# Kernel optimization log

Measured on AMD Instinct MI355X. Metric: run time of the kernel, lower is better.

## Reference

```python
import jax, jax.numpy as jnp
import numpy as np

BS, C, H, W = 8, 128, 64, 64
CH = C // 2  # proj output channels


def setup_inputs() -> dict:
    key = jax.random.key(0)
    ks = jax.random.split(key, 8)
    s = 1.0 / np.sqrt(C)
    return {
        "tgt": jax.random.normal(ks[0], (BS, C, H, W), dtype=jnp.float32),
        "ref": jax.random.normal(ks[1], (BS, C, H, W), dtype=jnp.float32),
        "W_tgt": jax.random.normal(ks[2], (CH, C), dtype=jnp.float32) * s,
        "b_tgt": jax.random.normal(ks[3], (CH,), dtype=jnp.float32) * s,
        "W_ref": jax.random.normal(ks[4], (CH, C), dtype=jnp.float32) * s,
        "b_ref": jax.random.normal(ks[5], (CH,), dtype=jnp.float32) * s,
        "W_out": jax.random.normal(ks[6], (C, C), dtype=jnp.float32) * s,
        "b_out": jax.random.normal(ks[7], (C,), dtype=jnp.float32) * s,
    }


def reference(tgt, ref, W_tgt, b_tgt, W_ref, b_ref, W_out, b_out):
    bs, c, h, w = tgt.shape
    n = h * w
    # 1x1 conv == per-pixel matmul over channels; flatten spatial to tokens
    tgt_f = tgt.reshape(bs, c, n)              # [bs, c, n]
    ref_f = ref.reshape(bs, c, n)              # [bs, c, n]
    # att_tgt: [bs, n, c/2] ; att_ref: [bs, c/2, n] (ReLU after proj)
    att_tgt = jax.nn.relu(jnp.einsum('bcn,oc->bno', tgt_f, W_tgt) + b_tgt)
    att_ref = jax.nn.relu(jnp.einsum('bcn,oc->bon', ref_f, W_ref) + b_ref[None, :, None])
    pre_att = jnp.einsum('bnd,bdm->bnm', att_tgt, att_ref)   # [bs, n, n]
    att = jax.nn.softmax(pre_att, axis=-1)
    # fused tokens: [bs, n, c] = att @ ref_tokens
    fused = jnp.einsum('bnm,bcm->bnc', att, ref_f)
    fused = fused.transpose(0, 2, 1).reshape(bs, c, h, w)
    # output gate: 1x1 conv on tgt (no activation), elementwise mul
    att_out = jnp.einsum('bcn,oc->bon', tgt_f, W_out) + b_out[None, :, None]
    fused = fused * att_out.reshape(bs, c, h, w)
    return fused
```

## Files before the change

### kernel.cpp

```cpp
#include <hip/hip_runtime.h>

typedef __attribute__((ext_vector_type(8))) _Float16 f16x8;
typedef __attribute__((ext_vector_type(4))) float f32x4;

constexpr int kC  = 128;
constexpr int kCH = 64;
constexpr int kN  = 4096;
constexpr float kLog2e = 1.4426950408889634f;

__device__ __forceinline__ unsigned pkrtz(float a, float b) {
    union { __fp16 __attribute__((ext_vector_type(2))) v; unsigned u; } cv;
    cv.v = __builtin_amdgcn_cvt_pkrtz(a, b);
    return cv.u;
}

__device__ __forceinline__ float x2(float x) {
    return __builtin_amdgcn_exp2f(x);
}

__device__ __forceinline__ void g2l16(const unsigned short* g, unsigned short* l) {
    __builtin_amdgcn_global_load_lds(
        (const __attribute__((address_space(1))) unsigned int*)(g),
        (__attribute__((address_space(3))) unsigned int*)(l),
        16, 0, 0);
}

__global__ __launch_bounds__(256, 4) void proj_mfma(
    const float* __restrict__ tgt, const float* __restrict__ ref,
    const float* __restrict__ Wt, const float* __restrict__ Wr,
    const float* __restrict__ Wo, const float* __restrict__ bt,
    const float* __restrict__ br, const float* __restrict__ bo,
    unsigned short* __restrict__ Qw, unsigned short* __restrict__ Kw,
    unsigned short* __restrict__ Vw, float* __restrict__ Gw)
{
    __shared__ __align__(16) unsigned short Xs[64 * 128];
    const int t = threadIdx.x;
    const int slice = blockIdx.y >> 3;
    const int b = blockIdx.y & 7;
    const int tokb = blockIdx.x << 6;

    const int w = t >> 6, lane = t & 63;
    const int lg = (lane >> 4) & 3, lm = lane & 15;

    const float* X = (slice == 1) ? ref : tgt;
    const float* Xb = X + ((size_t)b * kC) * kN + tokb;
    unsigned short* Vout = Vw + ((size_t)b * kC) * kN + tokb;

    const int tk4 = (t & 15) * 4;
    const int c8  = (t >> 4) * 8;
    f32x4 xv[8];
    #pragma unroll
    for (int j = 0; j < 8; ++j)
        xv[j] = *(const f32x4*)(Xb + (size_t)(c8 + j) * kN + tk4);

    f16x8 wf[2][4];
    float bvv[2][4];
    if (slice == 2) {
        const int ocb = w * 32;
        #pragma unroll
        for (int ot = 0; ot < 2; ++ot) {
            const int oc = ocb + ot * 16 + lm;
            #pragma unroll
            for (int ks = 0; ks < 4; ++ks) {
                const float* wp = Wo + (size_t)oc * kC + ks * 32 + lg * 8;
                f32x4 f0 = *(const f32x4*)wp;
                f32x4 f1 = *(const f32x4*)(wp + 4);
                union { f16x8 h; uint4 u; } cv;
                cv.u = make_uint4(pkrtz(f0[0], f0[1]), pkrtz(f0[2], f0[3]),
                                  pkrtz(f1[0], f1[1]), pkrtz(f1[2], f1[3]));
                wf[ot][ks] = cv.h;
            }
            #pragma unroll
            for (int r = 0; r < 4; ++r) bvv[ot][r] = bo[ocb + ot * 16 + lg * 4 + r];
        }
    } else {
        const float* W    = slice ? Wr : Wt;
        const float* bias = slice ? br : bt;
        const float scale = slice ? 1.0f : kLog2e;
        const int ocb = w * 16;
        #pragma unroll
        for (int ks = 0; ks < 4; ++ks) {
            const float* wp = W + (size_t)(ocb + lm) * kC + ks * 32 + lg * 8;
            f32x4 f0 = *(const f32x4*)wp;
            f32x4 f1 = *(const f32x4*)(wp + 4);
            union { f16x8 h; uint4 u; } cv;
            cv.u = make_uint4(pkrtz(f0[0] * scale, f0[1] * scale),
                              pkrtz(f0[2] * scale, f0[3] * scale),
                              pkrtz(f1[0] * scale, f1[1] * scale),
                              pkrtz(f1[2] * scale, f1[3] * scale));
            wf[0][ks] = cv.h;
        }
        #pragma unroll
        for (int r = 0; r < 4; ++r) bvv[0][r] = bias[ocb + lg * 4 + r] * scale;
    }

    if (slice == 1) {
        #pragma unroll
        for (int j = 0; j < 8; ++j)
            *(uint2*)(Vout + (size_t)(c8 + j) * kN + tk4) =
                make_uint2(pkrtz(xv[j][0], xv[j][1]), pkrtz(xv[j][2], xv[j][3]));
    }
    #pragma unroll
    for (int s = 0; s < 4; ++s) {
        const int tok = tk4 + s;
        const int cc = (c8 >> 3) ^ (tok & 7);
        uint4 pk;
        pk.x = pkrtz(xv[0][s], xv[1][s]);
        pk.y = pkrtz(xv[2][s], xv[3][s]);
        pk.z = pkrtz(xv[4][s], xv[5][s]);
        pk.w = pkrtz(xv[6][s], xv[7][s]);
        *(uint4*)(Xs + tok * 128 + cc * 8) = pk;
    }
    __syncthreads();

    if (slice == 2) {
        const int ocb = w * 32;
        float* Gb = Gw + ((size_t)b * kC) * kN + tokb;
        #pragma unroll
        for (int ns = 0; ns < 4; ++ns) {
            const int tok = ns * 16 + lm;
            f16x8 xf[4];
            #pragma unroll
            for (int ks = 0; ks < 4; ++ks)
                xf[ks] = *(const f16x8*)(Xs + tok * 128 +
                                         (((ks * 4 + lg) ^ (tok & 7)) << 3));
            #pragma unroll
            for (int ot = 0; ot < 2; ++ot) {
                f32x4 acc = {bvv[ot][0], bvv[ot][1], bvv[ot][2], bvv[ot][3]};
                #pragma unroll
                for (int ks = 0; ks < 4; ++ks)
                    acc = __builtin_amdgcn_mfma_f32_16x16x32_f16(wf[ot][ks], xf[ks], acc, 0, 0, 0);
                #pragma unroll
                for (int r = 0; r < 4; ++r)
                    Gb[(size_t)(ocb + ot * 16 + lg * 4 + r) * kN + tok] = acc[r];
            }
        }
    } else {
        const int ocb = w * 16;
        unsigned short* outp = (slice ? Kw : Qw) + ((size_t)b * kN + tokb) * kCH;
        #pragma unroll
        for (int ns = 0; ns < 4; ++ns) {
            const int tok = ns * 16 + lm;
            f16x8 xf[4];
            #pragma unroll
            for (int ks = 0; ks < 4; ++ks)
                xf[ks] = *(const f16x8*)(Xs + tok * 128 +
                                         (((ks * 4 + lg) ^ (tok & 7)) << 3));
            f32x4 acc = {bvv[0][0], bvv[0][1], bvv[0][2], bvv[0][3]};
            #pragma unroll
            for (int ks = 0; ks < 4; ++ks)
                acc = __builtin_amdgcn_mfma_f32_16x16x32_f16(wf[0][ks], xf[ks], acc, 0, 0, 0);
            uint2 pk;
            pk.x = pkrtz(fmaxf(acc[0], 0.f), fmaxf(acc[1], 0.f));
            pk.y = pkrtz(fmaxf(acc[2], 0.f), fmaxf(acc[3], 0.f));
            *(uint2*)(outp + (size_t)tok * kCH + ocb + lg * 4) = pk;
        }
    }
}

__global__ __launch_bounds__(256, 2) void flash7_kernel(
    const unsigned short* __restrict__ Qw,
    const unsigned short* __restrict__ Kw,
    const unsigned short* __restrict__ Vw,
    const float* __restrict__ Gw,
    float* __restrict__ out)
{
    __shared__ __align__(16) unsigned short Ks[2][64 * 64];
    __shared__ __align__(16) unsigned short Vs[2][128 * 64];
    __shared__ __align__(16) unsigned short Ps[64 * 64];

    const int t = threadIdx.x;
    const int b = blockIdx.x & 7;
    const int n0 = (blockIdx.x >> 3) << 6;
    const int w = t >> 6, lane = t & 63;
    const int lg = (lane >> 4) & 3, lm = lane & 15;
    const int row_q = w * 16 + lm;
    const int swz = lm & 7;

    const unsigned short* Qb = Qw + ((size_t)b * kN) * kCH;
    const unsigned short* Kb = Kw + ((size_t)b * kN) * kCH;
    const unsigned short* Vb = Vw + ((size_t)b * kC) * kN;

    f16x8 qf0 = *(const f16x8*)(Qb + (size_t)(n0 + row_q) * kCH + (lg << 3));
    f16x8 qf1 = *(const f16x8*)(Qb + (size_t)(n0 + row_q) * kCH + 32 + (lg << 3));

    const int srow = t >> 3, scol = t & 7;
    const int sco  = (scol ^ (srow & 7)) << 3;
    const int wv   = t >> 6;

    const int fswz0 = (lg ^ swz) << 3;
    const int fswz1 = ((4 | lg) ^ swz) << 3;
    int psw[4];
    #pragma unroll
    for (int mb = 0; mb < 4; ++mb)
        psw[mb] = row_q * 64 + (((2 * mb + (lg >> 1)) ^ swz) << 3) + ((lg & 1) << 2);

    union { f16x8 h; uint4 u; } onec;
    onec.u = make_uint4(0x3c003c00u, 0x3c003c00u, 0x3c003c00u, 0x3c003c00u);
    const f16x8 onev = onec.h;

    f32x4 O[8];
    #pragma unroll
    for (int cb = 0; cb < 8; ++cb) O[cb] = (f32x4){0.f, 0.f, 0.f, 0.f};
    f32x4 L = (f32x4){0.f, 0.f, 0.f, 0.f};
    float m_run = 0.0f;

    unsigned short* Ks0 = Ks[0]; unsigned short* Ks1 = Ks[1];
    unsigned short* Vs0 = Vs[0]; unsigned short* Vs1 = Vs[1];

    auto stage = [&](unsigned short* Kd, unsigned short* Vd, int m0) {
        g2l16(Kb + (size_t)(m0 + srow) * kCH + sco,      Kd + wv * 512);
        g2l16(Kb + (size_t)(m0 + 32 + srow) * kCH + sco, Kd + 2048 + wv * 512);
        #pragma unroll
        for (int j = 0; j < 4; ++j)
            g2l16(Vb + (size_t)(32 * j + srow) * kN + m0 + sco,
                  Vd + j * 2048 + wv * 512);
    };
    stage(Ks0, Vs0, 0);

    auto tile = [&](const unsigned short* Kc, const unsigned short* Vc,
                    unsigned short* Kn, unsigned short* Vn, int kt) {
        __syncthreads();
        if (kt + 1 < kN / 64) stage(Kn, Vn, (kt + 1) << 6);

        f32x4 s[4];
        __builtin_amdgcn_s_setprio(1);
        #pragma unroll
        for (int mb = 0; mb < 4; ++mb) {
            const unsigned short* kr = Kc + ((mb * 16 + lm) << 6);
            f16x8 kf0 = *(const f16x8*)(kr + fswz0);
            f16x8 kf1 = *(const f16x8*)(kr + fswz1);
            f32x4 acc = (f32x4){0.f, 0.f, 0.f, 0.f};
            acc = __builtin_amdgcn_mfma_f32_16x16x32_f16(kf0, qf0, acc, 0, 0, 0);
            acc = __builtin_amdgcn_mfma_f32_16x16x32_f16(kf1, qf1, acc, 0, 0, 0);
            s[mb] = acc;
        }
        __builtin_amdgcn_s_setprio(0);

        float mloc = 0.0f;
        #pragma unroll
        for (int mb = 0; mb < 4; ++mb)
            #pragma unroll
            for (int r = 0; r < 4; ++r) mloc = fmaxf(mloc, s[mb][r]);
        mloc = fmaxf(mloc, __shfl_xor(mloc, 16, 64));
        mloc = fmaxf(mloc, __shfl_xor(mloc, 32, 64));
        const bool upd = __any(mloc > m_run);
        const float mnew = upd ? fmaxf(m_run, mloc) : m_run;

        #pragma unroll
        for (int mb = 0; mb < 4; ++mb) {
            unsigned plo = pkrtz(x2(s[mb][0] - mnew), x2(s[mb][1] - mnew));
            unsigned phi = pkrtz(x2(s[mb][2] - mnew), x2(s[mb][3] - mnew));
            *(uint2*)(Ps + psw[mb]) = make_uint2(plo, phi);
        }

        if (upd) {
            float alpha = x2(m_run - mnew);
            float a0 = __shfl(alpha, (lg << 2) + 0, 64);
            float a1 = __shfl(alpha, (lg << 2) + 1, 64);
            float a2 = __shfl(alpha, (lg << 2) + 2, 64);
            float a3 = __shfl(alpha, (lg << 2) + 3, 64);
            #pragma unroll
            for (int cb = 0; cb < 8; ++cb) {
                O[cb][0] *= a0; O[cb][1] *= a1; O[cb][2] *= a2; O[cb][3] *= a3;
            }
            L[0] *= a0; L[1] *= a1; L[2] *= a2; L[3] *= a3;
            m_run = mnew;
        }

        f16x8 pf0 = *(const f16x8*)(Ps + row_q * 64 + fswz0);
        f16x8 pf1 = *(const f16x8*)(Ps + row_q * 64 + fswz1);
        __builtin_amdgcn_s_setprio(1);
        L = __builtin_amdgcn_mfma_f32_16x16x32_f16(pf0, onev, L, 0, 0, 0);
        L = __builtin_amdgcn_mfma_f32_16x16x32_f16(pf1, onev, L, 0, 0, 0);
        #pragma unroll
        for (int cb = 0; cb < 8; ++cb) {
            const unsigned short* vr = Vc + ((cb * 16 + lm) << 6);
            f16x8 vf0 = *(const f16x8*)(vr + fswz0);
            f16x8 vf1 = *(const f16x8*)(vr + fswz1);
            O[cb] = __builtin_amdgcn_mfma_f32_16x16x32_f16(pf0, vf0, O[cb], 0, 0, 0);
            O[cb] = __builtin_amdgcn_mfma_f32_16x16x32_f16(pf1, vf1, O[cb], 0, 0, 0);
        }
        __builtin_amdgcn_s_setprio(0);
    };

    for (int kt = 0; kt < kN / 64; kt += 2) {
        tile(Ks0, Vs0, Ks1, Vs1, kt);
        tile(Ks1, Vs1, Ks0, Vs0, kt + 1);
    }

    const float i0 = 1.0f / L[0], i1 = 1.0f / L[1];
    const float i2 = 1.0f / L[2], i3 = 1.0f / L[3];
    const float* Gb = Gw + ((size_t)b * kC) * kN;
    float* Ob = out + ((size_t)b * kC) * kN;
    #pragma unroll
    for (int cb = 0; cb < 8; ++cb) {
        int c = cb * 16 + lm;
        size_t base = (size_t)c * kN + n0 + w * 16 + (lg << 2);
        float4 g = *(const float4*)(Gb + base);
        float4 res;
        res.x = O[cb][0] * i0 * g.x;
        res.y = O[cb][1] * i1 * g.y;
        res.z = O[cb][2] * i2 * g.z;
        res.w = O[cb][3] * i3 * g.w;
        *(float4*)(Ob + base) = res;
    }
}

extern "C" void kernel_launch(void* const* d_in, const int* in_sizes, int n_in,
                              void* d_out, int out_size, void* d_ws, size_t ws_size,
                              hipStream_t stream) {
    const float* tgt   = (const float*)d_in[0];
    const float* ref   = (const float*)d_in[1];
    const float* W_tgt = (const float*)d_in[2];
    const float* b_tgt = (const float*)d_in[3];
    const float* W_ref = (const float*)d_in[4];
    const float* b_ref = (const float*)d_in[5];
    const float* W_out = (const float*)d_in[6];
    const float* b_out = (const float*)d_in[7];
    float* out = (float*)d_out;

    const size_t QK = (size_t)8 * kN * kCH;
    const size_t CV = (size_t)8 * kC * kN;
    unsigned short* Qw = (unsigned short*)d_ws;
    unsigned short* Kw = Qw + QK;
    unsigned short* Vw = Kw + QK;
    float*          Gw = (float*)(Vw + CV);

    proj_mfma<<<dim3(64, 24), 256, 0, stream>>>(tgt, ref, W_tgt, W_ref, W_out,
                                                b_tgt, b_ref, b_out, Qw, Kw, Vw, Gw);
    flash7_kernel<<<dim3(512), 256, 0, stream>>>(Qw, Kw, Vw, Gw, out);
}
```

Measured before the change: 186.8 us.

## Fuse Q and gate projections over shared tgt tile and double-buffer token tiles

```diff
diff --git a/kernel.cpp b/kernel.cpp
--- a/kernel.cpp
+++ b/kernel.cpp
@@ -25,7 +25,7 @@
         16, 0, 0);
 }
 
-__global__ __launch_bounds__(256, 4) void proj_mfma(
+__global__ __launch_bounds__(256, 2) void proj_fused(
     const float* __restrict__ tgt, const float* __restrict__ ref,
     const float* __restrict__ Wt, const float* __restrict__ Wr,
     const float* __restrict__ Wo, const float* __restrict__ bt,
@@ -33,29 +33,46 @@
     unsigned short* __restrict__ Qw, unsigned short* __restrict__ Kw,
     unsigned short* __restrict__ Vw, float* __restrict__ Gw)
 {
-    __shared__ __align__(16) unsigned short Xs[64 * 128];
+    __shared__ __align__(16) unsigned short Xs[2][64 * 128];
     const int t = threadIdx.x;
-    const int slice = blockIdx.y >> 3;
+    const int sl2 = blockIdx.y >> 3;
     const int b = blockIdx.y & 7;
-    const int tokb = blockIdx.x << 6;
+    const int tok0 = blockIdx.x << 7;
 
     const int w = t >> 6, lane = t & 63;
     const int lg = (lane >> 4) & 3, lm = lane & 15;
 
-    const float* X = (slice == 1) ? ref : tgt;
-    const float* Xb = X + ((size_t)b * kC) * kN + tokb;
-    unsigned short* Vout = Vw + ((size_t)b * kC) * kN + tokb;
-
-    const int tk4 = (t & 15) * 4;
-    const int c8  = (t >> 4) * 8;
-    f32x4 xv[8];
-    #pragma unroll
-    for (int j = 0; j < 8; ++j)
-        xv[j] = *(const f32x4*)(Xb + (size_t)(c8 + j) * kN + tk4);
-
-    f16x8 wf[2][4];
-    float bvv[2][4];
-    if (slice == 2) {
+    const float* X = sl2 ? ref : tgt;
+    const float* Xb0 = X + ((size_t)b * kC) * kN + tok0;
+    unsigned short* Vout = Vw + ((size_t)b * kC) * kN + tok0;
+
+    const float* Wqk  = sl2 ? Wr : Wt;
+    const float* bqk  = sl2 ? br : bt;
+    const float scale = sl2 ? 1.0f : kLog2e;
+
+    f16x8 wfq[4];
+    float bq[4];
+    {
+        const int ocb = w * 16;
+        #pragma unroll
+        for (int ks = 0; ks < 4; ++ks) {
+            const float* wp = Wqk + (size_t)(ocb + lm) * kC + ks * 32 + lg * 8;
+            f32x4 f0 = *(const f32x4*)wp;
+            f32x4 f1 = *(const f32x4*)(wp + 4);
+            union { f16x8 h; uint4 u; } cv;
+            cv.u = make_uint4(pkrtz(f0[0] * scale, f0[1] * scale),
+                              pkrtz(f0[2] * scale, f0[3] * scale),
+                              pkrtz(f1[0] * scale, f1[1] * scale),
+                              pkrtz(f1[2] * scale, f1[3] * scale));
+            wfq[ks] = cv.h;
+        }
+        #pragma unroll
+        for (int r = 0; r < 4; ++r) bq[r] = bqk[ocb + lg * 4 + r] * scale;
+    }
+
+    f16x8 wfg[2][4];
+    float bg[2][4];
+    if (sl2 == 0) {
         const int ocb = w * 32;
         #pragma unroll
         for (int ot = 0; ot < 2; ++ot) {
@@ -68,94 +85,87 @@
                 union { f16x8 h; uint4 u; } cv;
                 cv.u = make_uint4(pkrtz(f0[0], f0[1]), pkrtz(f0[2], f0[3]),
                                   pkrtz(f1[0], f1[1]), pkrtz(f1[2], f1[3]));
-                wf[ot][ks] = cv.h;
+                wfg[ot][ks] = cv.h;
             }
             #pragma unroll
-            for (int r = 0; r < 4; ++r) bvv[ot][r] = bo[ocb + ot * 16 + lg * 4 + r];
-        }
-    } else {
-        const float* W    = slice ? Wr : Wt;
-        const float* bias = slice ? br : bt;
-        const float scale = slice ? 1.0f : kLog2e;
-        const int ocb = w * 16;
-        #pragma unroll
-        for (int ks = 0; ks < 4; ++ks) {
-            const float* wp = W + (size_t)(ocb + lm) * kC + ks * 32 + lg * 8;
-            f32x4 f0 = *(const f32x4*)wp;
-            f32x4 f1 = *(const f32x4*)(wp + 4);
-            union { f16x8 h; uint4 u; } cv;
-            cv.u = make_uint4(pkrtz(f0[0] * scale, f0[1] * scale),
-                              pkrtz(f0[2] * scale, f0[3] * scale),
-                              pkrtz(f1[0] * scale, f1[1] * scale),
-                              pkrtz(f1[2] * scale, f1[3] * scale));
-            wf[0][ks] = cv.h;
-        }
-        #pragma unroll
-        for (int r = 0; r < 4; ++r) bvv[0][r] = bias[ocb + lg * 4 + r] * scale;
+            for (int r = 0; r < 4; ++r) bg[ot][r] = bo[ocb + ot * 16 + lg * 4 + r];
+        }
     }
 
-    if (slice == 1) {
+    const int tk4 = (t & 15) * 4;
+    const int c8  = (t >> 4) * 8;
+
+    auto loadX = [&](int toff, f32x4* xv) {
         #pragma unroll
         for (int j = 0; j < 8; ++j)
-            *(uint2*)(Vout + (size_t)(c8 + j) * kN + tk4) =
-                make_uint2(pkrtz(xv[j][0], xv[j][1]), pkrtz(xv[j][2], xv[j][3]));
-    }
-    #pragma unroll
-    for (int s = 0; s < 4; ++s) {
-        const int tok = tk4 + s;
-        const int cc = (c8 >> 3) ^ (tok & 7);
-        uint4 pk;
-        pk.x = pkrtz(xv[0][s], xv[1][s]);
-        pk.y = pkrtz(xv[2][s], xv[3][s]);
-        pk.z = pkrtz(xv[4][s], xv[5][s]);
-        pk.w = pkrtz(xv[6][s], xv[7][s]);
-        *(uint4*)(Xs + tok * 128 + cc * 8) = pk;
-    }
-    __syncthreads();
-
-    if (slice == 2) {
-        const int ocb = w * 32;
+            xv[j] = *(const f32x4*)(Xb0 + (size_t)(c8 + j) * kN + toff + tk4);
+    };
+    auto stageX = [&](const f32x4* xv, unsigned short* Xsb, int toff) {
+        if (sl2 == 1) {
+            #pragma unroll
+            for (int j = 0; j < 8; ++j)
+                *(uint2*)(Vout + (size_t)(c8 + j) * kN + toff + tk4) =
+                    make_uint2(pkrtz(xv[j][0], xv[j][1]), pkrtz(xv[j][2], xv[j][3]));
+        }
+        #pragma unroll
+        for (int s = 0; s < 4; ++s) {
+            const int tok = tk4 + s;
+            const int cc = (c8 >> 3) ^ (tok & 7);
+            uint4 pk;
+            pk.x = pkrtz(xv[0][s], xv[1][s]);
+            pk.y = pkrtz(xv[2][s], xv[3][s]);
+            pk.z = pkrtz(xv[4][s], xv[5][s]);
+            pk.w = pkrtz(xv[6][s], xv[7][s]);
+            *(uint4*)(Xsb + tok * 128 + cc * 8) = pk;
+        }
+    };
+    auto compute = [&](const unsigned short* Xsb, int tokb) {
+        unsigned short* outp = (sl2 ? Kw : Qw) + ((size_t)b * kN + tokb) * kCH;
         float* Gb = Gw + ((size_t)b * kC) * kN + tokb;
+        const int ocq = w * 16;
+        const int ocg = w * 32;
         #pragma unroll
         for (int ns = 0; ns < 4; ++ns) {
             const int tok = ns * 16 + lm;
             f16x8 xf[4];
             #pragma unroll
             for (int ks = 0; ks < 4; ++ks)
-                xf[ks] = *(const f16x8*)(Xs + tok * 128 +
+                xf[ks] = *(const f16x8*)(Xsb + tok * 128 +
                                          (((ks * 4 + lg) ^ (tok & 7)) << 3));
-            #pragma unroll
-            for (int ot = 0; ot < 2; ++ot) {
-                f32x4 acc = {bvv[ot][0], bvv[ot][1], bvv[ot][2], bvv[ot][3]};
+            {
+                f32x4 acc = {bq[0], bq[1], bq[2], bq[3]};
                 #pragma unroll
                 for (int ks = 0; ks < 4; ++ks)
-                    acc = __builtin_amdgcn_mfma_f32_16x16x32_f16(wf[ot][ks], xf[ks], acc, 0, 0, 0);
+                    acc = __builtin_amdgcn_mfma_f32_16x16x32_f16(wfq[ks], xf[ks], acc, 0, 0, 0);
+                uint2 pk;
+                pk.x = pkrtz(fmaxf(acc[0], 0.f), fmaxf(acc[1], 0.f));
+                pk.y = pkrtz(fmaxf(acc[2], 0.f), fmaxf(acc[3], 0.f));
+                *(uint2*)(outp + (size_t)tok * kCH + ocq + lg * 4) = pk;
+            }
+            if (sl2 == 0) {
                 #pragma unroll
-                for (int r = 0; r < 4; ++r)
-                    Gb[(size_t)(ocb + ot * 16 + lg * 4 + r) * kN + tok] = acc[r];
+                for (int ot = 0; ot < 2; ++ot) {
+                    f32x4 acc = {bg[ot][0], bg[ot][1], bg[ot][2], bg[ot][3]};
+                    #pragma unroll
+                    for (int ks = 0; ks < 4; ++ks)
+                        acc = __builtin_amdgcn_mfma_f32_16x16x32_f16(wfg[ot][ks], xf[ks], acc, 0, 0, 0);
+                    #pragma unroll
+                    for (int r = 0; r < 4; ++r)
+                        Gb[(size_t)(ocg + ot * 16 + lg * 4 + r) * kN + tok] = acc[r];
+                }
             }
         }
-    } else {
-        const int ocb = w * 16;
-        unsigned short* outp = (slice ? Kw : Qw) + ((size_t)b * kN + tokb) * kCH;
-        #pragma unroll
-        for (int ns = 0; ns < 4; ++ns) {
-            const int tok = ns * 16 + lm;
-            f16x8 xf[4];
-            #pragma unroll
-            for (int ks = 0; ks < 4; ++ks)
-                xf[ks] = *(const f16x8*)(Xs + tok * 128 +
-                                         (((ks * 4 + lg) ^ (tok & 7)) << 3));
-            f32x4 acc = {bvv[0][0], bvv[0][1], bvv[0][2], bvv[0][3]};
-            #pragma unroll
-            for (int ks = 0; ks < 4; ++ks)
-                acc = __builtin_amdgcn_mfma_f32_16x16x32_f16(wf[0][ks], xf[ks], acc, 0, 0, 0);
-            uint2 pk;
-            pk.x = pkrtz(fmaxf(acc[0], 0.f), fmaxf(acc[1], 0.f));
-            pk.y = pkrtz(fmaxf(acc[2], 0.f), fmaxf(acc[3], 0.f));
-            *(uint2*)(outp + (size_t)tok * kCH + ocb + lg * 4) = pk;
-        }
-    }
+    };
+
+    f32x4 xv[8], xw[8];
+    loadX(0, xv);
+    stageX(xv, Xs[0], 0);
+    __syncthreads();
+    loadX(64, xw);
+    compute(Xs[0], tok0);
+    stageX(xw, Xs[1], 64);
+    __syncthreads();
+    compute(Xs[1], tok0 + 64);
 }
 
 __global__ __launch_bounds__(256, 2) void flash7_kernel(
@@ -327,7 +337,7 @@
     unsigned short* Vw = Kw + QK;
     float*          Gw = (float*)(Vw + CV);
 
-    proj_mfma<<<dim3(64, 24), 256, 0, stream>>>(tgt, ref, W_tgt, W_ref, W_out,
-                                                b_tgt, b_ref, b_out, Qw, Kw, Vw, Gw);
+    proj_fused<<<dim3(32, 16), 256, 0, stream>>>(tgt, ref, W_tgt, W_ref, W_out,
+                                                 b_tgt, b_ref, b_out, Qw, Kw, Vw, Gw);
     flash7_kernel<<<dim3(512), 256, 0, stream>>>(Qw, Kw, Vw, Gw, out);
 }
```

Result: no change. 183.4 us (-1.8%).

## Fuse query projection and output gate into flash attention kernel

Applied to the files above, without the earlier changes.

```diff
diff --git a/kernel.cpp b/kernel.cpp
--- a/kernel.cpp
+++ b/kernel.cpp
@@ -25,25 +25,26 @@
         16, 0, 0);
 }
 
-__global__ __launch_bounds__(256, 4) void proj_mfma(
-    const float* __restrict__ tgt, const float* __restrict__ ref,
-    const float* __restrict__ Wt, const float* __restrict__ Wr,
-    const float* __restrict__ Wo, const float* __restrict__ bt,
-    const float* __restrict__ br, const float* __restrict__ bo,
-    unsigned short* __restrict__ Qw, unsigned short* __restrict__ Kw,
-    unsigned short* __restrict__ Vw, float* __restrict__ Gw)
+__device__ __forceinline__ void lds_barrier() {
+    asm volatile("s_waitcnt lgkmcnt(0)" ::: "memory");
+    __builtin_amdgcn_sched_barrier(0);
+    __builtin_amdgcn_s_barrier();
+}
+
+__global__ __launch_bounds__(256, 2) void proj_kv(
+    const float* __restrict__ ref, const float* __restrict__ Wr,
+    const float* __restrict__ br, unsigned short* __restrict__ Kw,
+    unsigned short* __restrict__ Vw)
 {
     __shared__ __align__(16) unsigned short Xs[64 * 128];
     const int t = threadIdx.x;
-    const int slice = blockIdx.y >> 3;
-    const int b = blockIdx.y & 7;
+    const int b = blockIdx.y;
     const int tokb = blockIdx.x << 6;
 
     const int w = t >> 6, lane = t & 63;
     const int lg = (lane >> 4) & 3, lm = lane & 15;
 
-    const float* X = (slice == 1) ? ref : tgt;
-    const float* Xb = X + ((size_t)b * kC) * kN + tokb;
+    const float* Xb = ref + ((size_t)b * kC) * kN + tokb;
     unsigned short* Vout = Vw + ((size_t)b * kC) * kN + tokb;
 
     const int tk4 = (t & 15) * 4;
@@ -53,53 +54,26 @@
     for (int j = 0; j < 8; ++j)
         xv[j] = *(const f32x4*)(Xb + (size_t)(c8 + j) * kN + tk4);
 
-    f16x8 wf[2][4];
-    float bvv[2][4];
-    if (slice == 2) {
-        const int ocb = w * 32;
-        #pragma unroll
-        for (int ot = 0; ot < 2; ++ot) {
-            const int oc = ocb + ot * 16 + lm;
-            #pragma unroll
-            for (int ks = 0; ks < 4; ++ks) {
-                const float* wp = Wo + (size_t)oc * kC + ks * 32 + lg * 8;
-                f32x4 f0 = *(const f32x4*)wp;
-                f32x4 f1 = *(const f32x4*)(wp + 4);
-                union { f16x8 h; uint4 u; } cv;
-                cv.u = make_uint4(pkrtz(f0[0], f0[1]), pkrtz(f0[2], f0[3]),
-                                  pkrtz(f1[0], f1[1]), pkrtz(f1[2], f1[3]));
-                wf[ot][ks] = cv.h;
-            }
-            #pragma unroll
-            for (int r = 0; r < 4; ++r) bvv[ot][r] = bo[ocb + ot * 16 + lg * 4 + r];
-        }
-    } else {
-        const float* W    = slice ? Wr : Wt;
-        const float* bias = slice ? br : bt;
-        const float scale = slice ? 1.0f : kLog2e;
-        const int ocb = w * 16;
-        #pragma unroll
-        for (int ks = 0; ks < 4; ++ks) {
-            const float* wp = W + (size_t)(ocb + lm) * kC + ks * 32 + lg * 8;
-            f32x4 f0 = *(const f32x4*)wp;
-            f32x4 f1 = *(const f32x4*)(wp + 4);
-            union { f16x8 h; uint4 u; } cv;
-            cv.u = make_uint4(pkrtz(f0[0] * scale, f0[1] * scale),
-                              pkrtz(f0[2] * scale, f0[3] * scale),
-                              pkrtz(f1[0] * scale, f1[1] * scale),
-                              pkrtz(f1[2] * scale, f1[3] * scale));
-            wf[0][ks] = cv.h;
-        }
-        #pragma unroll
-        for (int r = 0; r < 4; ++r) bvv[0][r] = bias[ocb + lg * 4 + r] * scale;
-    }
-
-    if (slice == 1) {
-        #pragma unroll
-        for (int j = 0; j < 8; ++j)
-            *(uint2*)(Vout + (size_t)(c8 + j) * kN + tk4) =
-                make_uint2(pkrtz(xv[j][0], xv[j][1]), pkrtz(xv[j][2], xv[j][3]));
-    }
+    f16x8 wf[4];
+    float bq[4];
+    const int ocb = w * 16;
+    #pragma unroll
+    for (int ks = 0; ks < 4; ++ks) {
+        const float* wp = Wr + (size_t)(ocb + lm) * kC + ks * 32 + lg * 8;
+        f32x4 f0 = *(const f32x4*)wp;
+        f32x4 f1 = *(const f32x4*)(wp + 4);
+        union { f16x8 h; uint4 u; } cv;
+        cv.u = make_uint4(pkrtz(f0[0], f0[1]), pkrtz(f0[2], f0[3]),
+                          pkrtz(f1[0], f1[1]), pkrtz(f1[2], f1[3]));
+        wf[ks] = cv.h;
+    }
+    #pragma unroll
+    for (int r = 0; r < 4; ++r) bq[r] = br[ocb + lg * 4 + r];
+
+    #pragma unroll
+    for (int j = 0; j < 8; ++j)
+        *(uint2*)(Vout + (size_t)(c8 + j) * kN + tk4) =
+            make_uint2(pkrtz(xv[j][0], xv[j][1]), pkrtz(xv[j][2], xv[j][3]));
     #pragma unroll
     for (int s = 0; s < 4; ++s) {
         const int tok = tk4 + s;
@@ -113,56 +87,32 @@
     }
     __syncthreads();
 
-    if (slice == 2) {
-        const int ocb = w * 32;
-        float* Gb = Gw + ((size_t)b * kC) * kN + tokb;
-        #pragma unroll
-        for (int ns = 0; ns < 4; ++ns) {
-            const int tok = ns * 16 + lm;
-            f16x8 xf[4];
-            #pragma unroll
-            for (int ks = 0; ks < 4; ++ks)
-                xf[ks] = *(const f16x8*)(Xs + tok * 128 +
-                                         (((ks * 4 + lg) ^ (tok & 7)) << 3));
-            #pragma unroll
-            for (int ot = 0; ot < 2; ++ot) {
-                f32x4 acc = {bvv[ot][0], bvv[ot][1], bvv[ot][2], bvv[ot][3]};
-                #pragma unroll
-                for (int ks = 0; ks < 4; ++ks)
-                    acc = __builtin_amdgcn_mfma_f32_16x16x32_f16(wf[ot][ks], xf[ks], acc, 0, 0, 0);
-                #pragma unroll
-                for (int r = 0; r < 4; ++r)
-                    Gb[(size_t)(ocb + ot * 16 + lg * 4 + r) * kN + tok] = acc[r];
-            }
-        }
-    } else {
-        const int ocb = w * 16;
-        unsigned short* outp = (slice ? Kw : Qw) + ((size_t)b * kN + tokb) * kCH;
-        #pragma unroll
-        for (int ns = 0; ns < 4; ++ns) {
-            const int tok = ns * 16 + lm;
-            f16x8 xf[4];
-            #pragma unroll
-            for (int ks = 0; ks < 4; ++ks)
-                xf[ks] = *(const f16x8*)(Xs + tok * 128 +
-                                         (((ks * 4 + lg) ^ (tok & 7)) << 3));
-            f32x4 acc = {bvv[0][0], bvv[0][1], bvv[0][2], bvv[0][3]};
-            #pragma unroll
-            for (int ks = 0; ks < 4; ++ks)
-                acc = __builtin_amdgcn_mfma_f32_16x16x32_f16(wf[0][ks], xf[ks], acc, 0, 0, 0);
-            uint2 pk;
-            pk.x = pkrtz(fmaxf(acc[0], 0.f), fmaxf(acc[1], 0.f));
-            pk.y = pkrtz(fmaxf(acc[2], 0.f), fmaxf(acc[3], 0.f));
-            *(uint2*)(outp + (size_t)tok * kCH + ocb + lg * 4) = pk;
-        }
-    }
-}
-
-__global__ __launch_bounds__(256, 2) void flash7_kernel(
-    const unsigned short* __restrict__ Qw,
+    unsigned short* outp = Kw + ((size_t)b * kN + tokb) * kCH;
+    #pragma unroll
+    for (int ns = 0; ns < 4; ++ns) {
+        const int tok = ns * 16 + lm;
+        f16x8 xf[4];
+        #pragma unroll
+        for (int ks = 0; ks < 4; ++ks)
+            xf[ks] = *(const f16x8*)(Xs + tok * 128 +
+                                     (((ks * 4 + lg) ^ (tok & 7)) << 3));
+        f32x4 acc = {bq[0], bq[1], bq[2], bq[3]};
+        #pragma unroll
+        for (int ks = 0; ks < 4; ++ks)
+            acc = __builtin_amdgcn_mfma_f32_16x16x32_f16(wf[ks], xf[ks], acc, 0, 0, 0);
+        uint2 pk;
+        pk.x = pkrtz(fmaxf(acc[0], 0.f), fmaxf(acc[1], 0.f));
+        pk.y = pkrtz(fmaxf(acc[2], 0.f), fmaxf(acc[3], 0.f));
+        *(uint2*)(outp + (size_t)tok * kCH + ocb + lg * 4) = pk;
+    }
+}
+
+__global__ __launch_bounds__(256, 2) void flash9_kernel(
+    const float* __restrict__ tgt,
     const unsigned short* __restrict__ Kw,
     const unsigned short* __restrict__ Vw,
-    const float* __restrict__ Gw,
+    const float* __restrict__ Wt, const float* __restrict__ bt,
+    const float* __restrict__ Wo, const float* __restrict__ bo,
     float* __restrict__ out)
 {
     __shared__ __align__(16) unsigned short Ks[2][64 * 64];
@@ -177,12 +127,9 @@
     const int row_q = w * 16 + lm;
     const int swz = lm & 7;
 
-    const unsigned short* Qb = Qw + ((size_t)b * kN) * kCH;
     const unsigned short* Kb = Kw + ((size_t)b * kN) * kCH;
     const unsigned short* Vb = Vw + ((size_t)b * kC) * kN;
-
-    f16x8 qf0 = *(const f16x8*)(Qb + (size_t)(n0 + row_q) * kCH + (lg << 3));
-    f16x8 qf1 = *(const f16x8*)(Qb + (size_t)(n0 + row_q) * kCH + 32 + (lg << 3));
+    const float* Tb = tgt + ((size_t)b * kC) * kN + n0;
 
     const int srow = t >> 3, scol = t & 7;
     const int sco  = (scol ^ (srow & 7)) << 3;
@@ -217,6 +164,71 @@
                   Vd + j * 2048 + wv * 512);
     };
     stage(Ks0, Vs0, 0);
+
+    const int tk4 = (t & 15) * 4;
+    const int c8  = (t >> 4) * 8;
+
+    auto stageT = [&](unsigned short* Xs) {
+        f32x4 xv[8];
+        #pragma unroll
+        for (int j = 0; j < 8; ++j)
+            xv[j] = *(const f32x4*)(Tb + (size_t)(c8 + j) * kN + tk4);
+        #pragma unroll
+        for (int s = 0; s < 4; ++s) {
+            const int tok = tk4 + s;
+            const int cc = (c8 >> 3) ^ (tok & 7);
+            uint4 pk;
+            pk.x = pkrtz(xv[0][s], xv[1][s]);
+            pk.y = pkrtz(xv[2][s], xv[3][s]);
+            pk.z = pkrtz(xv[4][s], xv[5][s]);
+            pk.w = pkrtz(xv[6][s], xv[7][s]);
+            *(uint4*)(Xs + tok * 128 + cc * 8) = pk;
+        }
+    };
+
+    f16x8 qf0, qf1;
+    {
+        f16x8 wq[4];
+        float bq4[4];
+        #pragma unroll
+        for (int ks = 0; ks < 4; ++ks) {
+            const float* wp = Wt + (size_t)(w * 16 + lm) * kC + ks * 32 + lg * 8;
+            f32x4 f0 = *(const f32x4*)wp;
+            f32x4 f1 = *(const f32x4*)(wp + 4);
+            union { f16x8 h; uint4 u; } cv;
+            cv.u = make_uint4(pkrtz(f0[0] * kLog2e, f0[1] * kLog2e),
+                              pkrtz(f0[2] * kLog2e, f0[3] * kLog2e),
+                              pkrtz(f1[0] * kLog2e, f1[1] * kLog2e),
+                              pkrtz(f1[2] * kLog2e, f1[3] * kLog2e));
+            wq[ks] = cv.h;
+        }
+        #pragma unroll
+        for (int r = 0; r < 4; ++r) bq4[r] = bt[w * 16 + lg * 4 + r] * kLog2e;
+
+        stageT(Vs1);
+        lds_barrier();
+
+        const int qsw = lm * 64 + (((2 * w + (lg >> 1)) ^ (lm & 7)) << 3) + ((lg & 1) << 2);
+        #pragma unroll
+        for (int ns = 0; ns < 4; ++ns) {
+            const int tok = ns * 16 + lm;
+            f16x8 xf[4];
+            #pragma unroll
+            for (int ks = 0; ks < 4; ++ks)
+                xf[ks] = *(const f16x8*)(Vs1 + tok * 128 +
+                                         (((ks * 4 + lg) ^ (tok & 7)) << 3));
+            f32x4 acc = {bq4[0], bq4[1], bq4[2], bq4[3]};
+            #pragma unroll
+            for (int ks = 0; ks < 4; ++ks)
+                acc = __builtin_amdgcn_mfma_f32_16x16x32_f16(wq[ks], xf[ks], acc, 0, 0, 0);
+            *(uint2*)(Ps + qsw + ns * 1024) = make_uint2(
+                pkrtz(fmaxf(acc[0], 0.f), fmaxf(acc[1], 0.f)),
+                pkrtz(fmaxf(acc[2], 0.f), fmaxf(acc[3], 0.f)));
+        }
+        lds_barrier();
+        qf0 = *(const f16x8*)(Ps + row_q * 64 + fswz0);
+        qf1 = *(const f16x8*)(Ps + row_q * 64 + fswz1);
+    }
 
     auto tile = [&](const unsigned short* Kc, const unsigned short* Vc,
                     unsigned short* Kn, unsigned short* Vn, int kt) {
@@ -289,20 +301,45 @@
         tile(Ks1, Vs1, Ks0, Vs0, kt + 1);
     }
 
+    __syncthreads();
+    stageT(Vs0);
+    __syncthreads();
+
     const float i0 = 1.0f / L[0], i1 = 1.0f / L[1];
     const float i2 = 1.0f / L[2], i3 = 1.0f / L[3];
-    const float* Gb = Gw + ((size_t)b * kC) * kN;
     float* Ob = out + ((size_t)b * kC) * kN;
+
+    f16x8 tf[4];
+    #pragma unroll
+    for (int ks = 0; ks < 4; ++ks)
+        tf[ks] = *(const f16x8*)(Vs0 + row_q * 128 + (((ks * 4 + lg) ^ swz) << 3));
+
     #pragma unroll
     for (int cb = 0; cb < 8; ++cb) {
-        int c = cb * 16 + lm;
+        const int c = cb * 16 + lm;
+        f16x8 wo[4];
+        #pragma unroll
+        for (int ks = 0; ks < 4; ++ks) {
+            const float* wp = Wo + (size_t)c * kC + ks * 32 + lg * 8;
+            f32x4 f0 = *(const f32x4*)wp;
+            f32x4 f1 = *(const f32x4*)(wp + 4);
+            union { f16x8 h; uint4 u; } cv;
+            cv.u = make_uint4(pkrtz(f0[0], f0[1]), pkrtz(f0[2], f0[3]),
+                              pkrtz(f1[0], f1[1]), pkrtz(f1[2], f1[3]));
+            wo[ks] = cv.h;
+        }
+        const float bc = bo[c];
+        f32x4 g = {bc, bc, bc, bc};
+        #pragma unroll
+        for (int ks = 0; ks < 4; ++ks)
+            g = __builtin_amdgcn_mfma_f32_16x16x32_f16(tf[ks], wo[ks], g, 0, 0, 0);
+
         size_t base = (size_t)c * kN + n0 + w * 16 + (lg << 2);
-        float4 g = *(const float4*)(Gb + base);
         float4 res;
-        res.x = O[cb][0] * i0 * g.x;
-        res.y = O[cb][1] * i1 * g.y;
-        res.z = O[cb][2] * i2 * g.z;
-        res.w = O[cb][3] * i3 * g.w;
+        res.x = O[cb][0] * i0 * g[0];
+        res.y = O[cb][1] * i1 * g[1];
+        res.z = O[cb][2] * i2 * g[2];
+        res.w = O[cb][3] * i3 * g[3];
         *(float4*)(Ob + base) = res;
     }
 }
@@ -321,13 +358,10 @@
     float* out = (float*)d_out;
 
     const size_t QK = (size_t)8 * kN * kCH;
-    const size_t CV = (size_t)8 * kC * kN;
-    unsigned short* Qw = (unsigned short*)d_ws;
-    unsigned short* Kw = Qw + QK;
+    unsigned short* Kw = (unsigned short*)d_ws;
     unsigned short* Vw = Kw + QK;
-    float*          Gw = (float*)(Vw + CV);
-
-    proj_mfma<<<dim3(64, 24), 256, 0, stream>>>(tgt, ref, W_tgt, W_ref, W_out,
-                                                b_tgt, b_ref, b_out, Qw, Kw, Vw, Gw);
-    flash7_kernel<<<dim3(512), 256, 0, stream>>>(Qw, Kw, Vw, Gw, out);
-}
+
+    proj_kv<<<dim3(64, 8), 256, 0, stream>>>(ref, W_ref, b_ref, Kw, Vw);
+    flash9_kernel<<<dim3(512), 256, 0, stream>>>(tgt, Kw, Vw, W_tgt, b_tgt,
+                                                 W_out, b_out, out);
+}
```

After: 195.3 us. 1.05x slower.
